# Performance work log

Hardware: AMD Instinct MI355X
Metric: run time of the kernel (lower is better)

Reference implementation:

```python
import jax, jax.numpy as jnp
import numpy as np

N_NODES, N_PARENTS, K_WORDS, MAX_DEG = 16384, 8192, 32, 4
VOCAB, HID, NCLASS = 100000, 64, 4
NEG_INF = -1e30


def setup_inputs() -> dict:
    key = jax.random.key(0)
    ks = jax.random.split(key, 16)
    L = N_NODES - N_PARENTS
    # tree: leaves-first node ordering; parent i is node L+i, children are earlier nodes
    rng = np.random.default_rng(0)
    tree = np.full((N_PARENTS, MAX_DEG + 1), -1, dtype=np.int32)
    for i in range(N_PARENTS):
        hi = L + i
        nc = int(rng.integers(1, MAX_DEG + 1))
        ch = rng.choice(hi, size=min(nc, hi), replace=False)
        tree[i, :len(ch)] = ch
        tree[i, MAX_DEG] = hi  # parent slot, ignored (row[:-1] used)
    s = 0.1
    return {
        "x_word": jax.random.uniform(ks[0], (N_NODES, K_WORDS), jnp.float32),
        "x_index": jax.random.randint(ks[1], (N_NODES, K_WORDS), 0, VOCAB, jnp.int32),
        "tree": jnp.asarray(tree),
        "E_bu": s * jax.random.normal(ks[2], (HID, VOCAB), jnp.float32),
        "W_z_bu": s * jax.random.normal(ks[3], (HID, HID), jnp.float32),
        "U_z_bu": s * jax.random.normal(ks[4], (HID, HID), jnp.float32),
        "b_z_bu": jnp.zeros((1, HID), jnp.float32),
        "W_r_bu": s * jax.random.normal(ks[5], (HID, HID), jnp.float32),
        "U_r_bu": s * jax.random.normal(ks[6], (HID, HID), jnp.float32),
        "b_r_bu": jnp.zeros((1, HID), jnp.float32),
        "W_h_bu": s * jax.random.normal(ks[7], (HID, HID), jnp.float32),
        "U_h_bu": s * jax.random.normal(ks[8], (HID, HID), jnp.float32),
        "b_h_bu": jnp.zeros((1, HID), jnp.float32),
        "W_attn": s * jax.random.normal(ks[9], (HID, HID), jnp.float32),
        "W_out_bu": s * jax.random.normal(ks[10], (NCLASS, HID), jnp.float32),
        "b_out_bu": jnp.zeros((NCLASS,), jnp.float32),
    }


def reference(x_word, x_index, tree, E_bu, W_z_bu, U_z_bu, b_z_bu,
              W_r_bu, U_r_bu, b_r_bu, W_h_bu, U_h_bu, b_h_bu,
              W_attn, W_out_bu, b_out_bu):
    N = x_word.shape[0]
    P = tree.shape[0]
    L = N - P  # leaves first
    H = E_bu.shape[0]
    # node embedding xe[n] = x_word[n] @ E_bu[:, x_index[n]].T  -> [N,H]
    Eg = E_bu.T[x_index]                       # [N,K,H] gather (memory-bound)
    xe = jnp.einsum('nk,nkh->nh', x_word, Eg)  # [N,H]
    # Leaf update: child_h = zeros -> attn uniform, h_tilde = 0
    z_l = jax.nn.sigmoid(xe[:L] @ W_z_bu.T + b_z_bu)
    c_l = jnp.tanh(xe[:L] @ W_h_bu.T + b_h_bu)
    leaf_h = (1.0 - z_l) * c_l                 # z*0 + (1-z)*c
    node_h0 = jnp.zeros((N, H), xe.dtype).at[:L].set(leaf_h)
    children = tree[:, :-1]                    # [P, D] child indices, -1 padded

    def step(node_h, inp):
        idx, ch = inp
        mask = ch > -1
        ci = jnp.where(mask, ch, 0)
        child_h = node_h[ci]                   # [D,H]
        pxe = xe[L + idx]                      # [H]
        # attn = softmax(sigmoid(parent_xe @ W_attn @ child_h.T)) over valid children
        logits = jax.nn.sigmoid(pxe @ (W_attn @ child_h.T))
        attn = jax.nn.softmax(jnp.where(mask, logits, NEG_INF))
        h_tilde = attn @ child_h               # [H]  (LayerNorm output discarded in original)
        z = jax.nn.sigmoid(pxe @ W_z_bu.T + h_tilde @ U_z_bu.T + b_z_bu[0])
        r = jax.nn.sigmoid(pxe @ W_r_bu.T + h_tilde @ U_r_bu.T + b_r_bu[0])
        c = jnp.tanh(pxe @ W_h_bu.T + (r * h_tilde) @ U_h_bu.T + b_h_bu[0])
        h = z * h_tilde + (1.0 - z) * c        # dropout in eval = identity
        return node_h.at[L + idx].set(h), None

    node_h, _ = jax.lax.scan(step, node_h0, (jnp.arange(P), children))
    final = jnp.max(node_h[L:], axis=0)        # [H]
    return jax.nn.softmax((W_out_bu * final).sum(axis=1) + b_out_bu)
```

## Files before the change

### kernel.cpp

```cpp
#include <hip/hip_runtime.h>
#include <math.h>

#define NN 16384
#define NP 8192
#define NL 8192
#define KW 32
#define VC 100000
#define SENT 0xFFFFFFFFu
#define CLEAN_EPOCH 1000

__device__ __forceinline__ float sigmoidf_(float x){ return 1.0f/(1.0f+expf(-x)); }

__global__ void __launch_bounds__(256) k_setup(const float* __restrict__ E, float* __restrict__ ET,
    const float* __restrict__ Wz, const float* __restrict__ Wr, const float* __restrict__ Wh,
    const float* __restrict__ Uz, const float* __restrict__ Ur, const float* __restrict__ Uh,
    float* __restrict__ WT, int* done, int* g_rem, int et_blocks){
  __shared__ float tile[64][65];
  int b = blockIdx.x;
  int lane = threadIdx.x & 63, ty = threadIdx.x >> 6;
  if (b < et_blocks){
    int v0 = b*64;
    for (int h = ty; h < 64; h += 4){
      int v = v0 + lane;
      tile[h][lane] = (v < VC) ? E[(size_t)h*VC + v] : 0.f;
    }
    __syncthreads();
    for (int vv = ty; vv < 64; vv += 4){
      int v = v0 + vv;
      if (v < VC) ET[v*64 + lane] = tile[lane][vv];
    }
  } else if (b < et_blocks + 6){
    int m = b - et_blocks;
    const float* src = (m==0)?Wz:(m==1)?Wr:(m==2)?Wh:(m==3)?Uz:(m==4)?Ur:Uh;
    float* dst = WT + m*4096;
    for (int h = ty; h < 64; h += 4) tile[h][lane] = src[h*64 + lane];
    __syncthreads();
    for (int k = ty; k < 64; k += 4) dst[k*64 + lane] = tile[lane][k];
  } else {
    int idx = (b - et_blocks - 6)*256 + threadIdx.x;
    if (idx < NP) done[idx] = 0;
    if (idx == 0) *g_rem = NP;
  }
}

__global__ void k_xe(const float* __restrict__ xw, const int* __restrict__ xi,
                     const float* __restrict__ ET, float* __restrict__ xe){
  int wid = blockIdx.x*(blockDim.x>>6) + (threadIdx.x>>6);
  int lane = threadIdx.x & 63;
  if (wid >= NN) return;
  int   idxl = (lane < KW) ? xi[wid*KW + lane] : 0;
  float wl   = (lane < KW) ? xw[wid*KW + lane] : 0.f;
  float acc = 0.f;
  #pragma unroll 8
  for (int k = 0; k < KW; ++k){
    int   vk = __shfl(idxl, k);
    float wk = __shfl(wl,   k);
    acc += wk * ET[vk*64 + lane];
  }
  xe[wid*64 + lane] = acc;
}

__global__ void k_xe_direct(const float* __restrict__ xw, const int* __restrict__ xi,
                            const float* __restrict__ E, float* __restrict__ xe){
  int wid = blockIdx.x*(blockDim.x>>6) + (threadIdx.x>>6);
  int lane = threadIdx.x & 63;
  if (wid >= NN) return;
  const float* w = xw + wid*KW;
  const int*   v = xi + wid*KW;
  const float* Erow = E + (size_t)lane*VC;
  float acc = 0.f;
  for (int k = 0; k < KW; ++k) acc += w[k] * Erow[v[k]];
  xe[wid*64 + lane] = acc;
}

__global__ void __launch_bounds__(256) k_node(const float* __restrict__ xe,
    const float* __restrict__ WzT, const float* __restrict__ WrT,
    const float* __restrict__ WhT, const float* __restrict__ Wa,
    const float* __restrict__ bz, const float* __restrict__ br,
    const float* __restrict__ bh,
    float* __restrict__ node_h, float* __restrict__ pz, float* __restrict__ pr,
    float* __restrict__ pc, float* __restrict__ qa){
  int wid = blockIdx.x*(blockDim.x>>6) + (threadIdx.x>>6);
  int lane = threadIdx.x & 63;
  if (wid >= NN) return;
  float xev = xe[wid*64 + lane];
  if (wid < NL){
    float az0=0.f, az1=0.f, ah0=0.f, ah1=0.f;
    #pragma unroll 8
    for (int k=0;k<64;k+=2){
      float x0 = __shfl(xev, k), x1 = __shfl(xev, k+1);
      az0 += x0 * WzT[k*64+lane];     az1 += x1 * WzT[(k+1)*64+lane];
      ah0 += x0 * WhT[k*64+lane];     ah1 += x1 * WhT[(k+1)*64+lane];
    }
    float z = sigmoidf_(az0+az1 + bz[lane]);
    float c = tanhf(ah0+ah1 + bh[lane]);
    node_h[wid*64+lane] = (1.f-z)*c;
  } else {
    int i = wid - NL;
    float az=0.f, ar=0.f, ah=0.f, aq=0.f;
    #pragma unroll 4
    for (int k=0;k<64;++k){
      float xk = __shfl(xev, k);
      az += xk * WzT[k*64+lane];
      ar += xk * WrT[k*64+lane];
      ah += xk * WhT[k*64+lane];
      aq += xk * Wa [k*64+lane];
    }
    pz[i*64+lane] = az + bz[lane];
    pr[i*64+lane] = ar + br[lane];
    pc[i*64+lane] = ah + bh[lane];
    qa[i*64+lane] = aq;
  }
}

__device__ __forceinline__ float gru_compute(int lane,
    int c0,int c1,int c2,int c3,
    float chv0,float chv1,float chv2,float chv3,
    float q, float pzv, float prv, float pcv,
    const float* __restrict__ UzT, const float* __restrict__ UrT,
    const float* __restrict__ UhT)
{
  float d0=q*chv0, d1=q*chv1, d2=q*chv2, d3=q*chv3;
  #pragma unroll
  for (int off=32; off; off>>=1){
    d0 += __shfl_xor(d0, off); d1 += __shfl_xor(d1, off);
    d2 += __shfl_xor(d2, off); d3 += __shfl_xor(d3, off);
  }
  float l0 = (c0>=0)? sigmoidf_(d0) : -1e30f;
  float l1 = (c1>=0)? sigmoidf_(d1) : -1e30f;
  float l2 = (c2>=0)? sigmoidf_(d2) : -1e30f;
  float l3 = (c3>=0)? sigmoidf_(d3) : -1e30f;
  float mx = fmaxf(fmaxf(l0,l1), fmaxf(l2,l3));
  float e0=expf(l0-mx), e1=expf(l1-mx), e2=expf(l2-mx), e3=expf(l3-mx);
  float inv = 1.f/(e0+e1+e2+e3);
  float ht = (e0*chv0 + e1*chv1 + e2*chv2 + e3*chv3)*inv;
  float az0=0.f, az1=0.f, ar0=0.f, ar1=0.f;
  #pragma unroll 8
  for (int k=0;k<64;k+=2){
    float h0 = __shfl(ht, k), h1 = __shfl(ht, k+1);
    az0 += h0 * UzT[k*64+lane];     az1 += h1 * UzT[(k+1)*64+lane];
    ar0 += h0 * UrT[k*64+lane];     ar1 += h1 * UrT[(k+1)*64+lane];
  }
  float z = sigmoidf_(pzv + az0+az1);
  float r = sigmoidf_(prv + ar0+ar1);
  float rh = r*ht;
  float ac0=0.f, ac1=0.f, ac2=0.f, ac3=0.f;
  #pragma unroll 8
  for (int k=0;k<64;k+=4){
    float r0 = __shfl(rh, k),   r1 = __shfl(rh, k+1);
    float r2 = __shfl(rh, k+2), r3 = __shfl(rh, k+3);
    ac0 += r0 * UhT[k*64+lane];     ac1 += r1 * UhT[(k+1)*64+lane];
    ac2 += r2 * UhT[(k+2)*64+lane]; ac3 += r3 * UhT[(k+3)*64+lane];
  }
  float cc = tanhf(pcv + (ac0+ac1)+(ac2+ac3));
  return z*ht + (1.f-z)*cc;
}

__global__ void __launch_bounds__(256) k_dflow(const int* __restrict__ tree,
    const float* __restrict__ qa, const float* __restrict__ pz,
    const float* __restrict__ pr, const float* __restrict__ pc,
    const float* __restrict__ UzT, const float* __restrict__ UrT,
    const float* __restrict__ UhT,
    float* node_h, int* done, int* g_rem)
{
  int w = threadIdx.x >> 6, lane = threadIdx.x & 63;
  int i = blockIdx.x*4 + w;
  if (i >= NP) return;
  const int* tr = tree + i*5;
  int c0=tr[0], c1=tr[1], c2=tr[2], c3=tr[3];
  float q   = qa[i*64+lane];
  float pzv = pz[i*64+lane];
  float prv = pr[i*64+lane];
  float pcv = pc[i*64+lane];
  unsigned int* nhu = (unsigned int*)node_h;
  float chv[4];
  bool ok = true;
  #pragma unroll
  for (int j=0;j<4;++j){
    int c = (j==0)?c0:(j==1)?c1:(j==2)?c2:c3;
    float v = 0.f;
    if (c >= 0 && c < NL){
      v = node_h[c*64+lane];
    } else if (c >= NL){
      unsigned int* p = &nhu[(size_t)c*64 + lane];
      unsigned int u = atomicCAS(p, SENT, SENT);
      int cnt = 0;
      while (__any((int)(u == SENT))){
        __builtin_amdgcn_s_sleep(32);
        u = atomicCAS(p, SENT, SENT);
        if (++cnt > (1<<15)) break;
      }
      if (__any((int)(u == SENT))){ ok = false; }
      v = __uint_as_float(u);
    }
    chv[j] = v;
  }
  if (!ok) return;
  float h = gru_compute(lane, c0,c1,c2,c3, chv[0],chv[1],chv[2],chv[3],
                        q, pzv, prv, pcv, UzT, UrT, UhT);
  atomicExch(&nhu[(size_t)(NL+i)*64 + lane], __float_as_uint(h));
  if (lane==0){ done[i] = 1; atomicAdd(g_rem, -1); }
}

__device__ __forceinline__ bool lvl_ready(int c, int lvl, const int* done){
  if (c < NL) return true;
  int e = done[c - NL];
  return (e > 0 && e < lvl);
}

__global__ void __launch_bounds__(256) k_cleanup(const int* __restrict__ tree,
    const float* __restrict__ qa, const float* __restrict__ pz,
    const float* __restrict__ pr, const float* __restrict__ pc,
    const float* __restrict__ UzT, const float* __restrict__ UrT,
    const float* __restrict__ UhT,
    float* node_h, int* done, int* g_rem)
{
  int rem = *g_rem;
  if (rem <= 0) return;
  __shared__ int cnt_s;
  int w = threadIdx.x >> 6, lane = threadIdx.x & 63;
  int epoch = CLEAN_EPOCH;
  while (rem > 0){
    if (threadIdx.x == 0) cnt_s = 0;
    __syncthreads();
    int my = 0;
    for (int i = w; i < NP; i += 4){
      if (done[i]) continue;
      const int* tr = tree + i*5;
      int c0=tr[0], c1=tr[1], c2=tr[2], c3=tr[3];
      if (!(lvl_ready(c0,epoch,done) && lvl_ready(c1,epoch,done)
         && lvl_ready(c2,epoch,done) && lvl_ready(c3,epoch,done))) continue;
      float chv0 = (c0>=0)? node_h[c0*64+lane] : 0.f;
      float chv1 = (c1>=0)? node_h[c1*64+lane] : 0.f;
      float chv2 = (c2>=0)? node_h[c2*64+lane] : 0.f;
      float chv3 = (c3>=0)? node_h[c3*64+lane] : 0.f;
      float h = gru_compute(lane, c0,c1,c2,c3, chv0,chv1,chv2,chv3,
                            qa[i*64+lane], pz[i*64+lane], pr[i*64+lane], pc[i*64+lane],
                            UzT, UrT, UhT);
      node_h[(size_t)(NL+i)*64+lane] = h;
      if (lane==0) done[i] = epoch;
      ++my;
    }
    if (lane==0 && my) atomicAdd(&cnt_s, my);
    __syncthreads();
    rem -= cnt_s;
    ++epoch;
    __syncthreads();
  }
}

__global__ void k_max1(const float* __restrict__ node_h, float* __restrict__ partial){
  __shared__ float sm[4][64];
  int lane = threadIdx.x & 63, w = threadIdx.x>>6;
  int base = NL + blockIdx.x*128;
  float m = -1e30f;
  for (int r = w; r < 128; r += 4)
    m = fmaxf(m, node_h[(size_t)(base+r)*64 + lane]);
  sm[w][lane] = m;
  __syncthreads();
  if (w==0){
    m = fmaxf(fmaxf(sm[0][lane],sm[1][lane]), fmaxf(sm[2][lane],sm[3][lane]));
    partial[blockIdx.x*64+lane] = m;
  }
}

__global__ void k_max2(const float* __restrict__ partial, const float* __restrict__ Wout,
                       const float* __restrict__ bout, float* __restrict__ out){
  int lane = threadIdx.x;
  float m = -1e30f;
  for (int b=0;b<64;++b) m = fmaxf(m, partial[b*64+lane]);
  float s0 = Wout[0*64+lane]*m;
  float s1 = Wout[1*64+lane]*m;
  float s2 = Wout[2*64+lane]*m;
  float s3 = Wout[3*64+lane]*m;
  #pragma unroll
  for (int off=32; off; off>>=1){
    s0 += __shfl_xor(s0, off);
    s1 += __shfl_xor(s1, off);
    s2 += __shfl_xor(s2, off);
    s3 += __shfl_xor(s3, off);
  }
  s0 += bout[0]; s1 += bout[1]; s2 += bout[2]; s3 += bout[3];
  float mx = fmaxf(fmaxf(s0,s1), fmaxf(s2,s3));
  float e0=expf(s0-mx), e1=expf(s1-mx), e2=expf(s2-mx), e3=expf(s3-mx);
  float inv = 1.f/(e0+e1+e2+e3);
  if (lane==0){
    out[0]=e0*inv; out[1]=e1*inv; out[2]=e2*inv; out[3]=e3*inv;
  }
}

__global__ void k_ws_sentinel(float* out, float wsmb){
  if (threadIdx.x < 4) out[threadIdx.x] = wsmb;
}

extern "C" void kernel_launch(void* const* d_in, const int* in_sizes, int n_in,
                              void* d_out, int out_size, void* d_ws, size_t ws_size,
                              hipStream_t stream){
  const float* x_word = (const float*)d_in[0];
  const int*   x_index= (const int*)d_in[1];
  const int*   tree   = (const int*)d_in[2];
  const float* E      = (const float*)d_in[3];
  const float* Wz     = (const float*)d_in[4];
  const float* Uz     = (const float*)d_in[5];
  const float* bz     = (const float*)d_in[6];
  const float* Wr     = (const float*)d_in[7];
  const float* Ur     = (const float*)d_in[8];
  const float* br     = (const float*)d_in[9];
  const float* Wh     = (const float*)d_in[10];
  const float* Uh     = (const float*)d_in[11];
  const float* bh     = (const float*)d_in[12];
  const float* Wa     = (const float*)d_in[13];
  const float* Wout   = (const float*)d_in[14];
  const float* bout   = (const float*)d_in[15];
  float* out = (float*)d_out;

  float* ws = (float*)d_ws;

  const size_t R0_FULL = 6400000;
  const size_t R0_FB   = 2101248;
  const size_t TAIL    = 1048576 + 1048576 + 24576 + NP + 1;
  const size_t FULL_NEED = (R0_FULL + TAIL) * 4;
  const size_t FB_NEED   = (R0_FB   + TAIL) * 4;

  bool full = (ws_size >= FULL_NEED);
  bool fb   = (!full && ws_size >= FB_NEED);
  if (!full && !fb){
    k_ws_sentinel<<<1, 64, 0, stream>>>(out, (float)(ws_size >> 20));
    return;
  }

  float* qa    = ws;
  float* pz    = qa + 524288;
  float* pr    = pz + 524288;
  float* pc    = pr + 524288;
  float* part  = pc + 524288;
  float* ET    = ws;
  size_t r0    = full ? R0_FULL : R0_FB;
  float* xe    = ws + r0;
  float* nodeh = xe + 1048576;
  float* WT    = nodeh + 1048576;
  int*   done  = (int*)(WT + 24576);
  int*   g_rem = done + NP;
  float* WzT = WT,       *WrT = WT+4096,  *WhT = WT+8192;
  float* UzT = WT+12288, *UrT = WT+16384, *UhT = WT+20480;

  hipMemsetAsync(nodeh + (size_t)NL*64, 0xFF, (size_t)NP*64*4, stream);

  int et_blocks = full ? (VC+63)/64 : 0;
  k_setup<<<et_blocks + 6 + NP/256, 256, 0, stream>>>(E, ET, Wz, Wr, Wh, Uz, Ur, Uh,
                                                      WT, done, g_rem, et_blocks);
  if (full) k_xe       <<<NN/4, 256, 0, stream>>>(x_word, x_index, ET, xe);
  else      k_xe_direct<<<NN/4, 256, 0, stream>>>(x_word, x_index, E, xe);
  k_node <<<NN/4, 256, 0, stream>>>(xe, WzT, WrT, WhT, Wa, bz, br, bh,
                                    nodeh, pz, pr, pc, qa);
  k_dflow<<<NP/4, 256, 0, stream>>>(tree, qa, pz, pr, pc, UzT, UrT, UhT,
                                    nodeh, done, g_rem);
  k_cleanup<<<1,  256, 0, stream>>>(tree, qa, pz, pr, pc, UzT, UrT, UhT,
                                    nodeh, done, g_rem);
  k_max1   <<<64, 256, 0, stream>>>(nodeh, part);
  k_max2   <<<1,   64, 0, stream>>>(part, Wout, bout, out);
}
```

Measured before the change: 202.5 us.

## Fuse embedding gather with node projections and cheapen dataflow child polling

Measured after the change: 184.0 us. 1.1x faster.

```diff
diff --git a/kernel.cpp b/kernel.cpp
--- a/kernel.cpp
+++ b/kernel.cpp
@@ -6,7 +6,8 @@
 #define NL 8192
 #define KW 32
 #define VC 100000
-#define SENT 0xFFFFFFFFu
+#define SENT  0xFFFFFFFFu
+#define NEVER 0xFFFFFFFEu
 #define CLEAN_EPOCH 1000
 
 __device__ __forceinline__ float sigmoidf_(float x){ return 1.0f/(1.0f+expf(-x)); }
@@ -14,7 +15,7 @@
 __global__ void __launch_bounds__(256) k_setup(const float* __restrict__ E, float* __restrict__ ET,
     const float* __restrict__ Wz, const float* __restrict__ Wr, const float* __restrict__ Wh,
     const float* __restrict__ Uz, const float* __restrict__ Ur, const float* __restrict__ Uh,
-    float* __restrict__ WT, int* done, int* g_rem, int et_blocks){
+    float* __restrict__ WT, float* __restrict__ node_h, int* done, int* g_rem, int et_blocks){
   __shared__ float tile[64][65];
   int b = blockIdx.x;
   int lane = threadIdx.x & 63, ty = threadIdx.x >> 6;
@@ -36,54 +37,23 @@
     for (int h = ty; h < 64; h += 4) tile[h][lane] = src[h*64 + lane];
     __syncthreads();
     for (int k = ty; k < 64; k += 4) dst[k*64 + lane] = tile[lane][k];
+  } else if (b < et_blocks + 6 + 2048){
+    size_t idx = (size_t)(b - et_blocks - 6)*256 + threadIdx.x;
+    ((unsigned int*)node_h)[(size_t)NL*64 + idx] = SENT;
   } else {
-    int idx = (b - et_blocks - 6)*256 + threadIdx.x;
+    int idx = (b - et_blocks - 6 - 2048)*256 + threadIdx.x;
     if (idx < NP) done[idx] = 0;
     if (idx == 0) *g_rem = NP;
   }
 }
 
-__global__ void k_xe(const float* __restrict__ xw, const int* __restrict__ xi,
-                     const float* __restrict__ ET, float* __restrict__ xe){
-  int wid = blockIdx.x*(blockDim.x>>6) + (threadIdx.x>>6);
-  int lane = threadIdx.x & 63;
-  if (wid >= NN) return;
-  int   idxl = (lane < KW) ? xi[wid*KW + lane] : 0;
-  float wl   = (lane < KW) ? xw[wid*KW + lane] : 0.f;
-  float acc = 0.f;
-  #pragma unroll 8
-  for (int k = 0; k < KW; ++k){
-    int   vk = __shfl(idxl, k);
-    float wk = __shfl(wl,   k);
-    acc += wk * ET[vk*64 + lane];
-  }
-  xe[wid*64 + lane] = acc;
-}
-
-__global__ void k_xe_direct(const float* __restrict__ xw, const int* __restrict__ xi,
-                            const float* __restrict__ E, float* __restrict__ xe){
-  int wid = blockIdx.x*(blockDim.x>>6) + (threadIdx.x>>6);
-  int lane = threadIdx.x & 63;
-  if (wid >= NN) return;
-  const float* w = xw + wid*KW;
-  const int*   v = xi + wid*KW;
-  const float* Erow = E + (size_t)lane*VC;
-  float acc = 0.f;
-  for (int k = 0; k < KW; ++k) acc += w[k] * Erow[v[k]];
-  xe[wid*64 + lane] = acc;
-}
-
-__global__ void __launch_bounds__(256) k_node(const float* __restrict__ xe,
+__device__ __forceinline__ void node_body(int wid, int lane, float xev,
     const float* __restrict__ WzT, const float* __restrict__ WrT,
     const float* __restrict__ WhT, const float* __restrict__ Wa,
     const float* __restrict__ bz, const float* __restrict__ br,
     const float* __restrict__ bh,
     float* __restrict__ node_h, float* __restrict__ pz, float* __restrict__ pr,
     float* __restrict__ pc, float* __restrict__ qa){
-  int wid = blockIdx.x*(blockDim.x>>6) + (threadIdx.x>>6);
-  int lane = threadIdx.x & 63;
-  if (wid >= NN) return;
-  float xev = xe[wid*64 + lane];
   if (wid < NL){
     float az0=0.f, az1=0.f, ah0=0.f, ah1=0.f;
     #pragma unroll 8
@@ -111,6 +81,48 @@
     pc[i*64+lane] = ah + bh[lane];
     qa[i*64+lane] = aq;
   }
+}
+
+__global__ void __launch_bounds__(256) k_xenode(const float* __restrict__ xw,
+    const int* __restrict__ xi, const float* __restrict__ ET,
+    const float* __restrict__ WzT, const float* __restrict__ WrT,
+    const float* __restrict__ WhT, const float* __restrict__ Wa,
+    const float* __restrict__ bz, const float* __restrict__ br,
+    const float* __restrict__ bh,
+    float* __restrict__ node_h, float* __restrict__ pz, float* __restrict__ pr,
+    float* __restrict__ pc, float* __restrict__ qa){
+  int wid = blockIdx.x*(blockDim.x>>6) + (threadIdx.x>>6);
+  int lane = threadIdx.x & 63;
+  if (wid >= NN) return;
+  int   idxl = (lane < KW) ? xi[wid*KW + lane] : 0;
+  float wl   = (lane < KW) ? xw[wid*KW + lane] : 0.f;
+  float xev = 0.f;
+  #pragma unroll 8
+  for (int k = 0; k < KW; ++k){
+    int   vk = __shfl(idxl, k);
+    float wk = __shfl(wl,   k);
+    xev += wk * ET[vk*64 + lane];
+  }
+  node_body(wid, lane, xev, WzT,WrT,WhT,Wa, bz,br,bh, node_h, pz,pr,pc, qa);
+}
+
+__global__ void __launch_bounds__(256) k_xenode_direct(const float* __restrict__ xw,
+    const int* __restrict__ xi, const float* __restrict__ E,
+    const float* __restrict__ WzT, const float* __restrict__ WrT,
+    const float* __restrict__ WhT, const float* __restrict__ Wa,
+    const float* __restrict__ bz, const float* __restrict__ br,
+    const float* __restrict__ bh,
+    float* __restrict__ node_h, float* __restrict__ pz, float* __restrict__ pr,
+    float* __restrict__ pc, float* __restrict__ qa){
+  int wid = blockIdx.x*(blockDim.x>>6) + (threadIdx.x>>6);
+  int lane = threadIdx.x & 63;
+  if (wid >= NN) return;
+  const float* w = xw + wid*KW;
+  const int*   v = xi + wid*KW;
+  const float* Erow = E + (size_t)lane*VC;
+  float xev = 0.f;
+  for (int k = 0; k < KW; ++k) xev += w[k] * Erow[v[k]];
+  node_body(wid, lane, xev, WzT,WrT,WhT,Wa, bz,br,bh, node_h, pz,pr,pc, qa);
 }
 
 __device__ __forceinline__ float gru_compute(int lane,
@@ -182,15 +194,22 @@
     if (c >= 0 && c < NL){
       v = node_h[c*64+lane];
     } else if (c >= NL){
-      unsigned int* p = &nhu[(size_t)c*64 + lane];
-      unsigned int u = atomicCAS(p, SENT, SENT);
-      int cnt = 0;
-      while (__any((int)(u == SENT))){
-        __builtin_amdgcn_s_sleep(32);
-        u = atomicCAS(p, SENT, SENT);
-        if (++cnt > (1<<15)) break;
+      unsigned int u = nhu[(size_t)c*64 + lane];
+      int rounds = 0;
+      while (__any((int)(u == SENT)) && rounds < (1<<16)){
+        if (lane == 0){
+          unsigned int s0 = atomicCAS(&nhu[(size_t)c*64], NEVER, NEVER);
+          while (s0 == SENT && rounds < (1<<16)){
+            __builtin_amdgcn_s_sleep(16);
+            ++rounds;
+            s0 = atomicCAS(&nhu[(size_t)c*64], NEVER, NEVER);
+          }
+        }
+        rounds = __shfl(rounds, 0) + 1;
+        if (u == SENT) u = atomicCAS(&nhu[(size_t)c*64 + lane], NEVER, NEVER);
+        if (__any((int)(u == SENT))) __builtin_amdgcn_s_sleep(4);
       }
-      if (__any((int)(u == SENT))){ ok = false; }
+      if (__any((int)(u == SENT))) ok = false;
       v = __uint_as_float(u);
     }
     chv[j] = v;
@@ -317,8 +336,8 @@
   float* ws = (float*)d_ws;
 
   const size_t R0_FULL = 6400000;
-  const size_t R0_FB   = 2101248;
-  const size_t TAIL    = 1048576 + 1048576 + 24576 + NP + 1;
+  const size_t R0_FB   = 4096;
+  const size_t TAIL    = 2097152 + 1048576 + 24576 + NP + 1;
   const size_t FULL_NEED = (R0_FULL + TAIL) * 4;
   const size_t FB_NEED   = (R0_FB   + TAIL) * 4;
 
@@ -329,34 +348,33 @@
     return;
   }
 
-  float* qa    = ws;
+  float* ET   = ws;
+  float* part = ws;
+  size_t r0   = full ? R0_FULL : R0_FB;
+  float* qa    = ws + r0;
   float* pz    = qa + 524288;
   float* pr    = pz + 524288;
   float* pc    = pr + 524288;
-  float* part  = pc + 524288;
-  float* ET    = ws;
-  size_t r0    = full ? R0_FULL : R0_FB;
-  float* xe    = ws + r0;
-  float* nodeh = xe + 1048576;
+  float* nodeh = pc + 524288;
   float* WT    = nodeh + 1048576;
   int*   done  = (int*)(WT + 24576);
   int*   g_rem = done + NP;
   float* WzT = WT,       *WrT = WT+4096,  *WhT = WT+8192;
   float* UzT = WT+12288, *UrT = WT+16384, *UhT = WT+20480;
 
-  hipMemsetAsync(nodeh + (size_t)NL*64, 0xFF, (size_t)NP*64*4, stream);
-
   int et_blocks = full ? (VC+63)/64 : 0;
-  k_setup<<<et_blocks + 6 + NP/256, 256, 0, stream>>>(E, ET, Wz, Wr, Wh, Uz, Ur, Uh,
-                                                      WT, done, g_rem, et_blocks);
-  if (full) k_xe       <<<NN/4, 256, 0, stream>>>(x_word, x_index, ET, xe);
-  else      k_xe_direct<<<NN/4, 256, 0, stream>>>(x_word, x_index, E, xe);
-  k_node <<<NN/4, 256, 0, stream>>>(xe, WzT, WrT, WhT, Wa, bz, br, bh,
-                                    nodeh, pz, pr, pc, qa);
-  k_dflow<<<NP/4, 256, 0, stream>>>(tree, qa, pz, pr, pc, UzT, UrT, UhT,
-                                    nodeh, done, g_rem);
-  k_cleanup<<<1,  256, 0, stream>>>(tree, qa, pz, pr, pc, UzT, UrT, UhT,
-                                    nodeh, done, g_rem);
-  k_max1   <<<64, 256, 0, stream>>>(nodeh, part);
-  k_max2   <<<1,   64, 0, stream>>>(part, Wout, bout, out);
-}
+  k_setup<<<et_blocks + 6 + 2048 + NP/256, 256, 0, stream>>>(
+      E, ET, Wz, Wr, Wh, Uz, Ur, Uh, WT, nodeh, done, g_rem, et_blocks);
+  if (full)
+    k_xenode<<<NN/4, 256, 0, stream>>>(x_word, x_index, ET, WzT, WrT, WhT, Wa,
+                                       bz, br, bh, nodeh, pz, pr, pc, qa);
+  else
+    k_xenode_direct<<<NN/4, 256, 0, stream>>>(x_word, x_index, E, WzT, WrT, WhT, Wa,
+                                              bz, br, bh, nodeh, pz, pr, pc, qa);
+  k_dflow  <<<NP/4, 256, 0, stream>>>(tree, qa, pz, pr, pc, UzT, UrT, UhT,
+                                      nodeh, done, g_rem);
+  k_cleanup<<<1,    256, 0, stream>>>(tree, qa, pz, pr, pc, UzT, UrT, UhT,
+                                      nodeh, done, g_rem);
+  k_max1   <<<64,   256, 0, stream>>>(nodeh, part);
+  k_max2   <<<1,     64, 0, stream>>>(part, Wout, bout, out);
+}
```
